# Kernel optimization log

Hardware: AMD Instinct MI355X
Metric: run time of the kernel (lower is better)

## Reference

```python
import jax, jax.numpy as jnp
import numpy as np

NODE_DIM = 64
DEPTH = 2
N = 50000          # node_size
DEG = 24           # average degree
E = N * DEG        # triple_size = 1.2M edges
R = 500            # rel_size
FEAT = NODE_DIM * (DEPTH + 1)  # 192


def _l2norm(x, eps=1e-12):
    # torch F.normalize(p=2): x / max(||x||, eps)
    n = jnp.sqrt(jnp.sum(x * x, axis=-1, keepdims=True))
    return x / jnp.maximum(n, eps)


def setup_inputs() -> dict:
    key = jax.random.key(0)
    ks = jax.random.split(key, 8)
    features = jax.random.normal(ks[0], (N, NODE_DIM), jnp.float32)
    rel_emb = jax.random.normal(ks[1], (R, NODE_DIM), jnp.float32)
    # duplicate-free edge list, rows sorted (matches a coalesced sparse adj)
    rows = jnp.repeat(jnp.arange(N, dtype=jnp.int32), DEG)
    offs = jnp.tile(1 + jnp.arange(DEG, dtype=jnp.int32) * 7, N)
    cols = (rows + offs) % N
    adj = jnp.stack([rows, cols])  # [2, E]
    # sparse [E, R] triple->relation matrix: one relation per triple
    r_index = jnp.stack([jnp.arange(E, dtype=jnp.int32),
                         jax.random.randint(ks[2], (E,), 0, R, jnp.int32)])
    r_val = jax.random.uniform(ks[3], (E,), jnp.float32, 0.5, 1.5)
    # params (xavier-ish scales)
    proxy = jax.random.normal(ks[4], (64, FEAT), jnp.float32) * (1.0 / np.sqrt(FEAT))
    gate_w = jax.random.normal(ks[5], (FEAT, FEAT), jnp.float32) * (1.0 / np.sqrt(FEAT))
    gate_b = jnp.zeros((FEAT,), jnp.float32)
    attn_kernels = jax.random.normal(ks[6], (DEPTH, NODE_DIM), jnp.float32) * 0.1
    return {"features": features, "rel_emb": rel_emb, "proxy": proxy,
            "gate_w": gate_w, "gate_b": gate_b, "attn_kernels": attn_kernels,
            "adj": adj, "r_index": r_index, "r_val": r_val,
            "triple_size": E, "rel_size": R, "node_size": N}


def reference(features, rel_emb, proxy, gate_w, gate_b, attn_kernels,
              adj, r_index, r_val, triple_size, rel_size, node_size):
    feats = jnp.tanh(features)
    outs = [feats]
    dst = adj[0]  # rows: softmax / scatter-sum segment ids
    src = adj[1]  # cols: neighbor gather ids
    for l in range(attn_kernels.shape[0]):
        neighs = feats[src]                                  # [E, d] gather
        # sparse.mm(tri_rel, rel_emb): sum_k r_val * rel_emb[rel_id] per triple
        tri_rel = jax.ops.segment_sum(r_val[:, None] * rel_emb[r_index[1]],
                                      r_index[0], num_segments=triple_size)
        tri_rel = _l2norm(tri_rel)                           # [E, d]
        # relational reflection: h - 2 <h, r> r
        neighs = neighs - 2.0 * jnp.sum(neighs * tri_rel, axis=1, keepdims=True) * tri_rel
        att = jnp.einsum('ed,d->e', tri_rel, attn_kernels[l])  # [E]
        # sparse softmax over rows of adjacency (segment softmax over dst)
        m = jax.ops.segment_max(att, dst, num_segments=node_size)
        ex = jnp.exp(att - m[dst])
        denom = jax.ops.segment_sum(ex, dst, num_segments=node_size)
        w = ex / denom[dst]
        new_f = jax.ops.segment_sum(neighs * w[:, None], dst, num_segments=node_size)
        feats = jnp.tanh(new_f)
        outs.append(feats)
    outputs = jnp.concatenate(outs, axis=-1)                 # [N, feat]
    proxy_att = jax.nn.softmax(_l2norm(outputs) @ _l2norm(proxy).T, axis=-1)
    proxy_feature = outputs - proxy_att @ proxy
    gate = jax.nn.sigmoid(proxy_feature @ gate_w.T + gate_b)
    return gate * outputs + (1.0 - gate) * proxy_feature
```

## Files before the change

kernel.cpp:

```cpp
#include <hip/hip_runtime.h>
#include <hip/hip_bf16.h>
#include <cstdint>
#include <cstddef>

#define N_NODES 50000
#define DEG     24
#define NEDGE   (N_NODES*DEG)
#define RSZ     500
#define NDIM    64
#define FEATD   192

#define LSTR    200

#define LGRID   1568
#define LCHUNK  196

typedef short bf16x8 __attribute__((ext_vector_type(8)));
typedef float f32x4  __attribute__((ext_vector_type(4)));

__device__ __forceinline__ unsigned short f2bf(float f) {
    unsigned u = __builtin_bit_cast(unsigned, f);
    unsigned r = (u + 0x7fffu + ((u >> 16) & 1u)) >> 16;
    return (unsigned short)r;
}
__device__ __forceinline__ float bf2f(unsigned short s) {
    unsigned u = ((unsigned)s) << 16;
    return __builtin_bit_cast(float, u);
}
__device__ __forceinline__ float lo16(unsigned u) {
    return __builtin_bit_cast(float, u << 16);
}
__device__ __forceinline__ float hi16(unsigned u) {
    return __builtin_bit_cast(float, u & 0xFFFF0000u);
}
__device__ __forceinline__ float fast_tanh(float x) {
    float e = __expf(2.f * x);
    return 1.f - 2.f / (e + 1.f);
}

__global__ __launch_bounds__(256) void k_prep(const float* __restrict__ features,
                                              const float* __restrict__ rel_emb,
                                              const float* __restrict__ attn_k,
                                              const float* __restrict__ proxy,
                                              const float* __restrict__ gate_w,
                                              const int* __restrict__ src,
                                              const int* __restrict__ rel,
                                              unsigned short* __restrict__ fin0,
                                              float* __restrict__ reln,
                                              float* __restrict__ expdot,
                                              float* __restrict__ pninv,
                                              unsigned short* __restrict__ B1,
                                              unsigned short* __restrict__ B2,
                                              unsigned short* __restrict__ B3,
                                              unsigned int* __restrict__ pedge) {
    int b = blockIdx.x;
    if (b < 3125) {
        int t = b * 256 + threadIdx.x;
        int idx4 = t * 4;
        float4 f = *reinterpret_cast<const float4*>(features + idx4);
        uint2 w;
        w.x = (unsigned)f2bf(fast_tanh(f.x)) | ((unsigned)f2bf(fast_tanh(f.y)) << 16);
        w.y = (unsigned)f2bf(fast_tanh(f.z)) | ((unsigned)f2bf(fast_tanh(f.w)) << 16);
        *reinterpret_cast<uint2*>(fin0 + idx4) = w;
    } else if (b < 3250) {
        int lane = threadIdx.x & 63;
        int row = (b - 3125) * 4 + (threadIdx.x >> 6);
        float v = rel_emb[row * 64 + lane];
        float ss = v * v;
        for (int m = 1; m < 64; m <<= 1) ss += __shfl_xor(ss, m);
        float inv = 1.f / fmaxf(sqrtf(ss), 1e-12f);
        float rn = v * inv;
        reln[row * 64 + lane] = rn;
        float d0 = rn * attn_k[lane];
        float d1 = rn * attn_k[64 + lane];
        for (int m = 1; m < 64; m <<= 1) { d0 += __shfl_xor(d0, m); d1 += __shfl_xor(d1, m); }
        if (lane == 0) { expdot[row] = __expf(d0); expdot[RSZ + row] = __expf(d1); }
    } else if (b < 3266) {
        int lane = threadIdx.x & 63;
        int row = (b - 3250) * 4 + (threadIdx.x >> 6);
        const float* p = proxy + (size_t)row * FEATD;
        float a = p[lane], bb = p[64 + lane], c = p[128 + lane];
        float ss = a * a + bb * bb + c * c;
        for (int m = 1; m < 64; m <<= 1) ss += __shfl_xor(ss, m);
        if (lane == 0) pninv[row] = 1.f / fmaxf(sqrtf(ss), 1e-12f);
    } else if (b < 3506) {
        int idx = (b - 3266) * 256 + threadIdx.x;
        int j = idx & 7, lane = (idx >> 3) & 63;
        int t = idx >> 9;
        int lane16 = lane & 15, quad = lane >> 4;
        if (t < 24) {
            int kt = t >> 2, nt = t & 3;
            int k = kt * 32 + quad * 8 + j, n = nt * 16 + lane16;
            B1[idx] = f2bf(proxy[(size_t)n * FEATD + k]);
        } else if (t < 48) {
            int tt = t - 24, kt = tt / 12, nt = tt % 12;
            int k = kt * 32 + quad * 8 + j, n = nt * 16 + lane16;
            B2[idx - 12288] = f2bf(proxy[(size_t)k * FEATD + n]);
        } else {
            int tt = t - 48, kt = tt / 12, nt = tt % 12;
            int k = kt * 32 + quad * 8 + j, n = nt * 16 + lane16;
            B3[idx - 24576] = f2bf(gate_w[(size_t)n * FEATD + k]);
        }
    } else {
        int t = (b - 3506) * 256 + threadIdx.x;
        if (t < NEDGE / 4) {
            int4 s4 = *reinterpret_cast<const int4*>(src + t * 4);
            int4 r4 = *reinterpret_cast<const int4*>(rel + t * 4);
            uint4 o;
            o.x = (unsigned)s4.x | ((unsigned)r4.x << 16);
            o.y = (unsigned)s4.y | ((unsigned)r4.y << 16);
            o.z = (unsigned)s4.z | ((unsigned)r4.z << 16);
            o.w = (unsigned)s4.w | ((unsigned)r4.w << 16);
            *reinterpret_cast<uint4*>(pedge + t * 4) = o;
        }
    }
}

__global__ __launch_bounds__(256) void k_layer(const unsigned int* __restrict__ pedge,
                                               const float* __restrict__ reln,
                                               const float* __restrict__ expdot_l,
                                               const unsigned short* __restrict__ fin,
                                               unsigned short* __restrict__ fout) {
    int b = blockIdx.x;
    int lb = (b & 7) * LCHUNK + (b >> 3);
    int lane8 = threadIdx.x & 7;
    int node = lb * 32 + (threadIdx.x >> 3);
    if (node >= N_NODES) return;
    int ebase = node * DEG;
    unsigned pk[DEG];
#pragma unroll
    for (int k = 0; k < DEG; k++) pk[k] = pedge[ebase + k];
    float a0 = 0.f, a1 = 0.f, a2 = 0.f, a3 = 0.f;
    float a4 = 0.f, a5 = 0.f, a6 = 0.f, a7 = 0.f, den = 0.f;
#pragma unroll 4
    for (int k = 0; k < DEG; k++) {
        unsigned p = pk[k];
        int s = p & 0xFFFF;
        int r = p >> 16;
        float ex = expdot_l[r];
        const float* tp = reln + (size_t)r * 64 + lane8 * 8;
        float4 t0 = *reinterpret_cast<const float4*>(tp);
        float4 t1v = *reinterpret_cast<const float4*>(tp + 4);
        uint4 u = *reinterpret_cast<const uint4*>(fin + (size_t)s * 64 + lane8 * 8);
        float n0 = lo16(u.x), n1 = hi16(u.x), n2 = lo16(u.y), n3 = hi16(u.y);
        float n4 = lo16(u.z), n5 = hi16(u.z), n6 = lo16(u.w), n7 = hi16(u.w);
        float pd = t0.x * n0 + t0.y * n1 + t0.z * n2 + t0.w * n3
                 + t1v.x * n4 + t1v.y * n5 + t1v.z * n6 + t1v.w * n7;
        pd += __shfl_xor(pd, 1); pd += __shfl_xor(pd, 2); pd += __shfl_xor(pd, 4);
        float t1 = -2.f * pd * ex;
        a0 = fmaf(ex, n0, fmaf(t1, t0.x, a0));
        a1 = fmaf(ex, n1, fmaf(t1, t0.y, a1));
        a2 = fmaf(ex, n2, fmaf(t1, t0.z, a2));
        a3 = fmaf(ex, n3, fmaf(t1, t0.w, a3));
        a4 = fmaf(ex, n4, fmaf(t1, t1v.x, a4));
        a5 = fmaf(ex, n5, fmaf(t1, t1v.y, a5));
        a6 = fmaf(ex, n6, fmaf(t1, t1v.z, a6));
        a7 = fmaf(ex, n7, fmaf(t1, t1v.w, a7));
        den += ex;
    }
    float id = 1.f / den;
    uint4 w;
    w.x = (unsigned)f2bf(fast_tanh(a0 * id)) | ((unsigned)f2bf(fast_tanh(a1 * id)) << 16);
    w.y = (unsigned)f2bf(fast_tanh(a2 * id)) | ((unsigned)f2bf(fast_tanh(a3 * id)) << 16);
    w.z = (unsigned)f2bf(fast_tanh(a4 * id)) | ((unsigned)f2bf(fast_tanh(a5 * id)) << 16);
    w.w = (unsigned)f2bf(fast_tanh(a6 * id)) | ((unsigned)f2bf(fast_tanh(a7 * id)) << 16);
    *reinterpret_cast<uint4*>(fout + (size_t)node * 64 + lane8 * 8) = w;
}

__global__ __launch_bounds__(256) void k_gate(const unsigned short* __restrict__ fin0,
                                              const unsigned short* __restrict__ fin1,
                                              const unsigned short* __restrict__ fin2,
                                              const unsigned short* __restrict__ B1,
                                              const unsigned short* __restrict__ B2,
                                              const unsigned short* __restrict__ B3,
                                              const float* __restrict__ pninv,
                                              const float* __restrict__ gate_b,
                                              float* __restrict__ dout) {
    __shared__ unsigned short lds[4][16 * LSTR];
    int wv = threadIdx.x >> 6, lane = threadIdx.x & 63;
    int tile = blockIdx.x * 4 + wv;
    if (tile > N_NODES / 16 - 1) tile = N_NODES / 16 - 1;
    int row0 = tile * 16, lane16 = lane & 15, quad = lane >> 4;
    unsigned short* L = lds[wv];
    const unsigned short* fsel[3] = {fin0, fin1, fin2};

    float oreg[12][4];
#pragma unroll
    for (int nt = 0; nt < 12; nt++) {
        const unsigned short* f = fsel[nt >> 2];
#pragma unroll
        for (int r = 0; r < 4; r++)
            oreg[nt][r] = bf2f(f[(size_t)(row0 + quad * 4 + r) * 64 + (nt & 3) * 16 + lane16]);
    }

    bf16x8 af[6];
    float ss = 0.f;
#pragma unroll
    for (int kt = 0; kt < 6; kt++) {
        const unsigned short* f = fsel[kt >> 1];
        bf16x8 a = *reinterpret_cast<const bf16x8*>(f + (size_t)(row0 + lane16) * 64 + (kt & 1) * 32 + quad * 8);
        af[kt] = a;
#pragma unroll
        for (int i = 0; i < 8; i++) {
            float v = bf2f((unsigned short)a[i]);
            ss = fmaf(v, v, ss);
        }
    }
    ss += __shfl_xor(ss, 16); ss += __shfl_xor(ss, 32);
    float inv = 1.f / fmaxf(sqrtf(ss), 1e-12f);
    float pni[4];
#pragma unroll
    for (int nt = 0; nt < 4; nt++) pni[nt] = pninv[nt * 16 + lane16];
    f32x4 acc4[4];
#pragma unroll
    for (int nt = 0; nt < 4; nt++) acc4[nt] = (f32x4){0.f, 0.f, 0.f, 0.f};
#pragma unroll
    for (int kt = 0; kt < 6; kt++) {
#pragma unroll
        for (int nt = 0; nt < 4; nt++) {
            bf16x8 bfr = *reinterpret_cast<const bf16x8*>(B1 + ((size_t)(kt * 4 + nt) * 64 + lane) * 8);
            acc4[nt] = __builtin_amdgcn_mfma_f32_16x16x32_bf16(af[kt], bfr, acc4[nt], 0, 0, 0);
        }
    }
#pragma unroll
    for (int r = 0; r < 4; r++) {
        int rowloc = quad * 4 + r;
        float invr = __shfl(inv, rowloc);
        float e0 = __expf(acc4[0][r] * invr * pni[0]);
        float e1 = __expf(acc4[1][r] * invr * pni[1]);
        float e2 = __expf(acc4[2][r] * invr * pni[2]);
        float e3 = __expf(acc4[3][r] * invr * pni[3]);
        float s = e0 + e1 + e2 + e3;
        s += __shfl_xor(s, 1); s += __shfl_xor(s, 2);
        s += __shfl_xor(s, 4); s += __shfl_xor(s, 8);
        float rs = 1.f / s;
        L[rowloc * LSTR + lane16]      = f2bf(e0 * rs);
        L[rowloc * LSTR + 16 + lane16] = f2bf(e1 * rs);
        L[rowloc * LSTR + 32 + lane16] = f2bf(e2 * rs);
        L[rowloc * LSTR + 48 + lane16] = f2bf(e3 * rs);
    }
    __threadfence_block();

    f32x4 acc[12];
#pragma unroll
    for (int nt = 0; nt < 12; nt++) acc[nt] = (f32x4){0.f, 0.f, 0.f, 0.f};
#pragma unroll
    for (int kt = 0; kt < 2; kt++) {
        bf16x8 a = *reinterpret_cast<const bf16x8*>(L + lane16 * LSTR + kt * 32 + quad * 8);
#pragma unroll
        for (int nt = 0; nt < 12; nt++) {
            bf16x8 bfr = *reinterpret_cast<const bf16x8*>(B2 + ((size_t)(kt * 12 + nt) * 64 + lane) * 8);
            acc[nt] = __builtin_amdgcn_mfma_f32_16x16x32_bf16(a, bfr, acc[nt], 0, 0, 0);
        }
    }
    __threadfence_block();
#pragma unroll
    for (int nt = 0; nt < 12; nt++) {
#pragma unroll
        for (int r = 0; r < 4; r++) {
            int rowloc = quad * 4 + r;
            L[rowloc * LSTR + nt * 16 + lane16] = f2bf(oreg[nt][r] - acc[nt][r]);
        }
    }
    __threadfence_block();

#pragma unroll
    for (int nt = 0; nt < 12; nt++) acc[nt] = (f32x4){0.f, 0.f, 0.f, 0.f};
#pragma unroll
    for (int kt = 0; kt < 6; kt++) {
        bf16x8 a = *reinterpret_cast<const bf16x8*>(L + lane16 * LSTR + kt * 32 + quad * 8);
#pragma unroll
        for (int nt = 0; nt < 12; nt++) {
            bf16x8 bfr = *reinterpret_cast<const bf16x8*>(B3 + ((size_t)(kt * 12 + nt) * 64 + lane) * 8);
            acc[nt] = __builtin_amdgcn_mfma_f32_16x16x32_bf16(a, bfr, acc[nt], 0, 0, 0);
        }
    }

#pragma unroll
    for (int nt = 0; nt < 12; nt++) {
        float bias = gate_b[nt * 16 + lane16];
#pragma unroll
        for (int r = 0; r < 4; r++) {
            int rowloc = quad * 4 + r;
            size_t idx = (size_t)(row0 + rowloc) * FEATD + nt * 16 + lane16;
            float z = acc[nt][r] + bias;
            float g = 1.f / (1.f + __expf(-z));
            float pf = bf2f(L[rowloc * LSTR + nt * 16 + lane16]);
            dout[idx] = pf + g * (oreg[nt][r] - pf);
        }
    }
}

extern "C" void kernel_launch(void* const* d_in, const int* in_sizes, int n_in,
                              void* d_out, int out_size, void* d_ws, size_t ws_size,
                              hipStream_t stream) {
    (void)in_sizes; (void)n_in; (void)out_size; (void)ws_size;
    const float* features = (const float*)d_in[0];
    const float* rel_emb  = (const float*)d_in[1];
    const float* proxy    = (const float*)d_in[2];
    const float* gate_w   = (const float*)d_in[3];
    const float* gate_b   = (const float*)d_in[4];
    const float* attn_k   = (const float*)d_in[5];
    const int*   adj      = (const int*)d_in[6];
    const int*   r_index  = (const int*)d_in[7];

    unsigned short* fin0 = (unsigned short*)d_ws;
    unsigned short* fin1 = fin0 + (size_t)N_NODES * 64;
    unsigned short* fin2 = fin1 + (size_t)N_NODES * 64;
    float* reln    = (float*)(fin2 + (size_t)N_NODES * 64);
    float* expdot  = reln + RSZ * 64;
    float* pninv   = expdot + 2 * RSZ;
    unsigned short* B1 = (unsigned short*)(pninv + 64);
    unsigned short* B2 = B1 + 12288;
    unsigned short* B3 = B2 + 12288;
    unsigned int* pedge = (unsigned int*)(B3 + 36864);

    const int* src = adj + NEDGE;
    const int* rel = r_index + NEDGE;

    k_prep  <<<dim3(4678), dim3(256), 0, stream>>>(features, rel_emb, attn_k, proxy, gate_w,
                                                   src, rel, fin0, reln, expdot,
                                                   pninv, B1, B2, B3, pedge);
    k_layer <<<dim3(LGRID), dim3(256), 0, stream>>>(pedge, reln, expdot,       fin0, fin1);
    k_layer <<<dim3(LGRID), dim3(256), 0, stream>>>(pedge, reln, expdot + RSZ, fin1, fin2);
    k_gate  <<<dim3(782),  dim3(256), 0, stream>>>(fin0, fin1, fin2, B1, B2, B3, pninv,
                                                   gate_b, (float*)d_out);
}
```

Measured before the change: 185.5 us.

## Fold proxy projection into gate GEMM via precomputed proxy·gate_w product

Rewrites the gate computation algebraically: gate pre-activation becomes outputs·W^T − att·(proxy·W^T), with proxy·W^T precomputed once in the prep kernel as a new bf16 B4 matrix. This removes the dependent chain of writing proxy_feature to LDS and re-reading it as the A operand, shrinks LDS to hold only the attention matrix, and processes output columns in chunks of 3 tiles to reduce register pressure from the old 48-float oreg array. The cost is extra small MFMAs per chunk and a slightly different bf16 rounding path, since proxy_feature is no longer materialized.

```diff
diff --git a/kernel.cpp b/kernel.cpp
--- a/kernel.cpp
+++ b/kernel.cpp
@@ -10,7 +10,7 @@
 #define NDIM    64
 #define FEATD   192
 
-#define LSTR    200
+#define PASTR   72
 
 #define LGRID   1568
 #define LCHUNK  196
@@ -52,6 +52,7 @@
                                               unsigned short* __restrict__ B1,
                                               unsigned short* __restrict__ B2,
                                               unsigned short* __restrict__ B3,
+                                              unsigned short* __restrict__ B4,
                                               unsigned int* __restrict__ pedge) {
     int b = blockIdx.x;
     if (b < 3125) {
@@ -101,7 +102,7 @@
             int k = kt * 32 + quad * 8 + j, n = nt * 16 + lane16;
             B3[idx - 24576] = f2bf(gate_w[(size_t)n * FEATD + k]);
         }
-    } else {
+    } else if (b < 4678) {
         int t = (b - 3506) * 256 + threadIdx.x;
         if (t < NEDGE / 4) {
             int4 s4 = *reinterpret_cast<const int4*>(src + t * 4);
@@ -113,6 +114,21 @@
             o.w = (unsigned)s4.w | ((unsigned)r4.w << 16);
             *reinterpret_cast<uint4*>(pedge + t * 4) = o;
         }
+    } else {
+        int t = (b - 4678) * 256 + threadIdx.x;
+        int j = t & 7, lane = (t >> 3) & 63, tl = t >> 9;
+        int lane16 = lane & 15, quad = lane >> 4;
+        int kt = tl / 12, nt = tl % 12;
+        int k = kt * 32 + quad * 8 + j, n = nt * 16 + lane16;
+        const float4* pr = reinterpret_cast<const float4*>(proxy + (size_t)k * FEATD);
+        const float4* gr = reinterpret_cast<const float4*>(gate_w + (size_t)n * FEATD);
+        float acc = 0.f;
+#pragma unroll 8
+        for (int q = 0; q < 48; q++) {
+            float4 a = pr[q], g4 = gr[q];
+            acc += a.x * g4.x + a.y * g4.y + a.z * g4.z + a.w * g4.w;
+        }
+        B4[t] = f2bf(acc);
     }
 }
 
@@ -173,25 +189,17 @@
                                               const unsigned short* __restrict__ B1,
                                               const unsigned short* __restrict__ B2,
                                               const unsigned short* __restrict__ B3,
+                                              const unsigned short* __restrict__ B4,
                                               const float* __restrict__ pninv,
                                               const float* __restrict__ gate_b,
                                               float* __restrict__ dout) {
-    __shared__ unsigned short lds[4][16 * LSTR];
+    __shared__ unsigned short lds[4][16 * PASTR];
     int wv = threadIdx.x >> 6, lane = threadIdx.x & 63;
     int tile = blockIdx.x * 4 + wv;
     if (tile > N_NODES / 16 - 1) tile = N_NODES / 16 - 1;
     int row0 = tile * 16, lane16 = lane & 15, quad = lane >> 4;
     unsigned short* L = lds[wv];
     const unsigned short* fsel[3] = {fin0, fin1, fin2};
-
-    float oreg[12][4];
-#pragma unroll
-    for (int nt = 0; nt < 12; nt++) {
-        const unsigned short* f = fsel[nt >> 2];
-#pragma unroll
-        for (int r = 0; r < 4; r++)
-            oreg[nt][r] = bf2f(f[(size_t)(row0 + quad * 4 + r) * 64 + (nt & 3) * 16 + lane16]);
-    }
 
     bf16x8 af[6];
     float ss = 0.f;
@@ -234,59 +242,65 @@
         s += __shfl_xor(s, 1); s += __shfl_xor(s, 2);
         s += __shfl_xor(s, 4); s += __shfl_xor(s, 8);
         float rs = 1.f / s;
-        L[rowloc * LSTR + lane16]      = f2bf(e0 * rs);
-        L[rowloc * LSTR + 16 + lane16] = f2bf(e1 * rs);
-        L[rowloc * LSTR + 32 + lane16] = f2bf(e2 * rs);
-        L[rowloc * LSTR + 48 + lane16] = f2bf(e3 * rs);
+        L[rowloc * PASTR + lane16]      = f2bf(e0 * rs);
+        L[rowloc * PASTR + 16 + lane16] = f2bf(e1 * rs);
+        L[rowloc * PASTR + 32 + lane16] = f2bf(e2 * rs);
+        L[rowloc * PASTR + 48 + lane16] = f2bf(e3 * rs);
     }
     __threadfence_block();
 
-    f32x4 acc[12];
-#pragma unroll
-    for (int nt = 0; nt < 12; nt++) acc[nt] = (f32x4){0.f, 0.f, 0.f, 0.f};
-#pragma unroll
-    for (int kt = 0; kt < 2; kt++) {
-        bf16x8 a = *reinterpret_cast<const bf16x8*>(L + lane16 * LSTR + kt * 32 + quad * 8);
-#pragma unroll
-        for (int nt = 0; nt < 12; nt++) {
-            bf16x8 bfr = *reinterpret_cast<const bf16x8*>(B2 + ((size_t)(kt * 12 + nt) * 64 + lane) * 8);
-            acc[nt] = __builtin_amdgcn_mfma_f32_16x16x32_bf16(a, bfr, acc[nt], 0, 0, 0);
-        }
-    }
-    __threadfence_block();
-#pragma unroll
-    for (int nt = 0; nt < 12; nt++) {
-#pragma unroll
-        for (int r = 0; r < 4; r++) {
-            int rowloc = quad * 4 + r;
-            L[rowloc * LSTR + nt * 16 + lane16] = f2bf(oreg[nt][r] - acc[nt][r]);
-        }
-    }
-    __threadfence_block();
-
-#pragma unroll
-    for (int nt = 0; nt < 12; nt++) acc[nt] = (f32x4){0.f, 0.f, 0.f, 0.f};
-#pragma unroll
-    for (int kt = 0; kt < 6; kt++) {
-        bf16x8 a = *reinterpret_cast<const bf16x8*>(L + lane16 * LSTR + kt * 32 + quad * 8);
-#pragma unroll
-        for (int nt = 0; nt < 12; nt++) {
-            bf16x8 bfr = *reinterpret_cast<const bf16x8*>(B3 + ((size_t)(kt * 12 + nt) * 64 + lane) * 8);
-            acc[nt] = __builtin_amdgcn_mfma_f32_16x16x32_bf16(a, bfr, acc[nt], 0, 0, 0);
-        }
-    }
-
-#pragma unroll
-    for (int nt = 0; nt < 12; nt++) {
-        float bias = gate_b[nt * 16 + lane16];
-#pragma unroll
-        for (int r = 0; r < 4; r++) {
-            int rowloc = quad * 4 + r;
-            size_t idx = (size_t)(row0 + rowloc) * FEATD + nt * 16 + lane16;
-            float z = acc[nt][r] + bias;
-            float g = 1.f / (1.f + __expf(-z));
-            float pf = bf2f(L[rowloc * LSTR + nt * 16 + lane16]);
-            dout[idx] = pf + g * (oreg[nt][r] - pf);
+    bf16x8 paf0 = *reinterpret_cast<const bf16x8*>(L + lane16 * PASTR + quad * 8);
+    bf16x8 paf1 = *reinterpret_cast<const bf16x8*>(L + lane16 * PASTR + 32 + quad * 8);
+
+#pragma unroll
+    for (int c = 0; c < 4; c++) {
+        int nt0 = c * 3;
+        f32x4 s3[3], s4[3], s2[3];
+#pragma unroll
+        for (int n = 0; n < 3; n++) {
+            s3[n] = (f32x4){0.f, 0.f, 0.f, 0.f};
+            s4[n] = (f32x4){0.f, 0.f, 0.f, 0.f};
+            s2[n] = (f32x4){0.f, 0.f, 0.f, 0.f};
+        }
+        float och[3][4];
+#pragma unroll
+        for (int n = 0; n < 3; n++) {
+            const unsigned short* f = fsel[(nt0 + n) >> 2];
+#pragma unroll
+            for (int r = 0; r < 4; r++)
+                och[n][r] = bf2f(f[(size_t)(row0 + quad * 4 + r) * 64 + ((nt0 + n) & 3) * 16 + lane16]);
+        }
+#pragma unroll
+        for (int kt = 0; kt < 6; kt++) {
+#pragma unroll
+            for (int n = 0; n < 3; n++) {
+                bf16x8 bfr = *reinterpret_cast<const bf16x8*>(B3 + ((size_t)(kt * 12 + nt0 + n) * 64 + lane) * 8);
+                s3[n] = __builtin_amdgcn_mfma_f32_16x16x32_bf16(af[kt], bfr, s3[n], 0, 0, 0);
+            }
+        }
+#pragma unroll
+        for (int n = 0; n < 3; n++) {
+            bf16x8 b40 = *reinterpret_cast<const bf16x8*>(B4 + ((size_t)(nt0 + n) * 64 + lane) * 8);
+            bf16x8 b41 = *reinterpret_cast<const bf16x8*>(B4 + ((size_t)(12 + nt0 + n) * 64 + lane) * 8);
+            s4[n] = __builtin_amdgcn_mfma_f32_16x16x32_bf16(paf0, b40, s4[n], 0, 0, 0);
+            s4[n] = __builtin_amdgcn_mfma_f32_16x16x32_bf16(paf1, b41, s4[n], 0, 0, 0);
+            bf16x8 b20 = *reinterpret_cast<const bf16x8*>(B2 + ((size_t)(nt0 + n) * 64 + lane) * 8);
+            bf16x8 b21 = *reinterpret_cast<const bf16x8*>(B2 + ((size_t)(12 + nt0 + n) * 64 + lane) * 8);
+            s2[n] = __builtin_amdgcn_mfma_f32_16x16x32_bf16(paf0, b20, s2[n], 0, 0, 0);
+            s2[n] = __builtin_amdgcn_mfma_f32_16x16x32_bf16(paf1, b21, s2[n], 0, 0, 0);
+        }
+#pragma unroll
+        for (int n = 0; n < 3; n++) {
+            int nt = nt0 + n;
+            float bias = gate_b[nt * 16 + lane16];
+#pragma unroll
+            for (int r = 0; r < 4; r++) {
+                int rowloc = quad * 4 + r;
+                float z = s3[n][r] - s4[n][r] + bias;
+                float g = 1.f / (1.f + __expf(-z));
+                dout[(size_t)(row0 + rowloc) * FEATD + nt * 16 + lane16] =
+                    och[n][r] - (1.f - g) * s2[n][r];
+            }
         }
     }
 }
@@ -313,16 +327,17 @@
     unsigned short* B1 = (unsigned short*)(pninv + 64);
     unsigned short* B2 = B1 + 12288;
     unsigned short* B3 = B2 + 12288;
-    unsigned int* pedge = (unsigned int*)(B3 + 36864);
+    unsigned short* B4 = B3 + 36864;
+    unsigned int* pedge = (unsigned int*)(B4 + 12288);
 
     const int* src = adj + NEDGE;
     const int* rel = r_index + NEDGE;
 
-    k_prep  <<<dim3(4678), dim3(256), 0, stream>>>(features, rel_emb, attn_k, proxy, gate_w,
+    k_prep  <<<dim3(4726), dim3(256), 0, stream>>>(features, rel_emb, attn_k, proxy, gate_w,
                                                    src, rel, fin0, reln, expdot,
-                                                   pninv, B1, B2, B3, pedge);
+                                                   pninv, B1, B2, B3, B4, pedge);
     k_layer <<<dim3(LGRID), dim3(256), 0, stream>>>(pedge, reln, expdot,       fin0, fin1);
     k_layer <<<dim3(LGRID), dim3(256), 0, stream>>>(pedge, reln, expdot + RSZ, fin1, fin2);
-    k_gate  <<<dim3(782),  dim3(256), 0, stream>>>(fin0, fin1, fin2, B1, B2, B3, pninv,
+    k_gate  <<<dim3(782),  dim3(256), 0, stream>>>(fin0, fin1, fin2, B1, B2, B3, B4, pninv,
                                                    gate_b, (float*)d_out);
 }
```

After: 191.7 us. 1.03x slower.
